# Kernel optimization log

Measured on AMD Instinct MI355X. Metric: run time of the kernel, lower is better.

Reference implementation:

```python
import jax, jax.numpy as jnp
import numpy as np

K = 32
D = 64
N_ITER = 10


def setup_inputs() -> dict:
    key = jax.random.key(0)
    k1, k2 = jax.random.split(key)
    B = 65536
    x = jax.random.normal(k1, (B, D), dtype=jnp.float32)
    c = jnp.zeros((K,), dtype=jnp.float32)
    mu = jax.random.normal(k2, (K, D), dtype=jnp.float32) * 0.1
    A = jnp.tile(jnp.eye(D, dtype=jnp.float32)[None], (K, 1, 1))
    alpha = jnp.float32(0.1)
    return {"x": x, "c": c, "mu": mu, "A": A, "alpha": alpha}


def _grad_phi(x, c, mu, A):
    # Precision matrices Sigma_i^{-1} = A_i^T A_i : (k, d, d)
    P = jnp.einsum('kji,kjl->kil', A, A)
    diff = x[:, None, :] - mu[None, :, :]          # (B, k, d)
    Pd = jnp.einsum('kij,bkj->bki', P, diff)       # Sigma^{-1} (x - mu)
    quad = jnp.einsum('bki,bki->bk', diff, Pd)     # (B, k)
    # Analytic gradient of phi(x) = logsumexp_i(c_i - 0.5 q_i):
    # grad = -sum_i softmax_i(c_i - 0.5 q_i) * Sigma_i^{-1}(x - mu_i)
    w = jax.nn.softmax(c[None, :] - 0.5 * quad, axis=1)  # (B, k)
    return -jnp.einsum('bk,bki->bi', w, Pd)


def reference(x, c, mu, A, alpha):
    def step(x_cur, _):
        x_new = x_cur + alpha * _grad_phi(x_cur, c, mu, A)
        return x_new, None
    x_final, _ = jax.lax.scan(step, x, None, length=N_ITER)
    return x_final
```

## Files before the change

kernel.cpp:

```cpp
#include <hip/hip_runtime.h>
#include <hip/hip_bf16.h>


typedef __attribute__((ext_vector_type(4))) float f32x4;
typedef __attribute__((ext_vector_type(8))) short bf16x8;

#define KC 32
#define NITER 10
#define XROW 72
#define WT_PITCH 40
#define PW_BYTES 7168
#define PSTG 8192
#define NBUF 4

static __device__ __forceinline__ unsigned pk_bf16(float a, float b) {
  __hip_bfloat16 ha = __float2bfloat16(a), hb = __float2bfloat16(b);
  unsigned short ua = *(unsigned short*)&ha, ub = *(unsigned short*)&hb;
  return (unsigned)ua | ((unsigned)ub << 16);
}

static __device__ __forceinline__ float red16(float x) {
#if __has_builtin(__builtin_amdgcn_permlane16_swap)
  int xi = __float_as_int(x);
  auto pr = __builtin_amdgcn_permlane16_swap(xi, xi, false, false);
  return __int_as_float(pr[0]) + __int_as_float(pr[1]);
#else
  int v = __builtin_amdgcn_ds_swizzle(__float_as_int(x), 0x401F);
  return x + __int_as_float(v);
#endif
}
static __device__ __forceinline__ float red32(float x) {
  int xi = __float_as_int(x);
  auto pr = __builtin_amdgcn_permlane32_swap(xi, xi, false, false);
  return __int_as_float(pr[0]) + __int_as_float(pr[1]);
}

static __device__ __forceinline__ void stage16(const void* gsrc, void* ldst) {
  __builtin_amdgcn_global_load_lds(
      (const __attribute__((address_space(1))) unsigned int*)gsrc,
      (__attribute__((address_space(3))) unsigned int*)ldst, 16, 0, 0);
}

__global__ void precompute1(const float* __restrict__ A, const float* __restrict__ mu,
                            const float* __restrict__ c,
                            float* __restrict__ Pmu_g, float* __restrict__ e_g,
                            __hip_bfloat16* __restrict__ Psw) {
  __shared__ float As[64 * 64];
  __shared__ float Pk[64 * 64];
  const int k = blockIdx.x, tid = threadIdx.x;
  const float* Ak = A + k * 4096;
  for (int idx = tid; idx < 1024; idx += 256)
    *(f32x4*)&As[idx * 4] = *(const f32x4*)&Ak[idx * 4];
  __syncthreads();

  const int i = tid >> 2, lg = tid & 3;
  float acc[16] = {};
  for (int j = 0; j < 64; ++j) {
    float ai = As[j * 64 + i];
    const f32x4* row = (const f32x4*)&As[j * 64 + lg * 16];
#pragma unroll
    for (int g = 0; g < 4; ++g) {
      f32x4 v = row[g];
#pragma unroll
      for (int r = 0; r < 4; ++r) acc[g * 4 + r] += ai * v[r];
    }
  }
#pragma unroll
  for (int g = 0; g < 4; ++g)
#pragma unroll
    for (int r = 0; r < 4; ++r) Pk[i * 64 + lg * 16 + g * 4 + r] = acc[g * 4 + r];
  __syncthreads();

  if (tid < 64) {
    float s = 0.f;
    for (int l = 0; l < 64; ++l) s += Pk[l * 64 + tid] * mu[k * 64 + l];
    Pmu_g[k * 64 + tid] = s;
    float v = mu[k * 64 + tid] * s;
#pragma unroll
    for (int off = 1; off < 64; off <<= 1) v += __shfl_xor(v, off, 64);
    if (tid == 0) e_g[k] = c[k] - 0.5f * v;
  }

  unsigned* Psw32 = (unsigned*)(Psw + k * 4096);
  for (int idx2 = tid; idx2 < 2048; idx2 += 256) {
    int idx = idx2 << 1;
    int f = idx >> 9, ln = (idx >> 3) & 63, j = idx & 7;
    int mt = f >> 1, s = f & 1, qq = ln >> 4, l4 = ln & 15;
    int col = mt * 16 + l4, rb = s * 32 + qq * 8 + j;
    Psw32[idx2] = pk_bf16(Pk[rb * 64 + col], Pk[(rb + 1) * 64 + col]);
  }
}

__global__ void precompute2(const float* __restrict__ Pmu_g,
                            __hip_bfloat16* __restrict__ PmuA,
                            __hip_bfloat16* __restrict__ PmuB) {
  const int tid = threadIdx.x;
  for (int idx = tid; idx < 2048; idx += 256) {
    int f = idx >> 9, lane = (idx >> 3) & 63, j = idx & 7;
    int mtc = f >> 1, s = f & 1, qq = lane >> 4, l4 = lane & 15;
    PmuA[idx] = __float2bfloat16(Pmu_g[(mtc * 16 + l4) * 64 + s * 32 + qq * 8 + j]);
  }
  for (int idx = tid; idx < 2048; idx += 256) {
    int f = idx >> 9, lane = (idx >> 3) & 63, j = idx & 7;
    int qq = lane >> 4, l4 = lane & 15;
    PmuB[idx] = __float2bfloat16(Pmu_g[(qq * 8 + j) * 64 + f * 16 + l4]);
  }
}

__launch_bounds__(256, 2)
__global__ void denoise_main(const float* __restrict__ x_in,
                             const float* __restrict__ e_g,
                             const float* __restrict__ alpha_g,
                             const __hip_bfloat16* __restrict__ Psw,
                             const __hip_bfloat16* __restrict__ PmuA,
                             const __hip_bfloat16* __restrict__ PmuB,
                             float* __restrict__ out) {
  __shared__ __attribute__((aligned(16))) char scratch[4 * PW_BYTES + NBUF * PSTG];

  const int tid = threadIdx.x;
  const int wave = tid >> 6, lane = tid & 63;
  const int q = lane >> 4, l4 = lane & 15;
  const int base_pt = blockIdx.x * 128 + wave * 32;
  const float alpha = alpha_g[0];

  char* pw = scratch + wave * PW_BYTES;
  __hip_bfloat16* xsw = (__hip_bfloat16*)pw;
  float* pmxw = (float*)pw;
  __hip_bfloat16* wtw = (__hip_bfloat16*)(pw + 4608);
  char* pstg = scratch + 4 * PW_BYTES;

  const char* PswB = (const char*)Psw;
  const bf16x8* PmuAF = (const bf16x8*)PmuA;
  const bf16x8* PmuBF = (const bf16x8*)PmuB;

  f32x4 xm[4][2];
#pragma unroll
  for (int mt = 0; mt < 4; ++mt)
#pragma unroll
    for (int nt = 0; nt < 2; ++nt)
      xm[mt][nt] = *(const f32x4*)&x_in[(base_pt + nt * 16 + l4) * 64 + mt * 16 + q * 4];

  f32x4 ev[2];
#pragma unroll
  for (int mtc = 0; mtc < 2; ++mtc) ev[mtc] = *(const f32x4*)&e_g[mtc * 16 + q * 4];

  const f32x4 Z4 = {0.f, 0.f, 0.f, 0.f};
  const int f0 = 2 * wave, f1 = 2 * wave + 1;

  stage16(PswB + f0 * 1024 + lane * 16, pstg + f0 * 1024);
  stage16(PswB + f1 * 1024 + lane * 16, pstg + f1 * 1024);
  stage16(PswB + PSTG + f0 * 1024 + lane * 16, pstg + PSTG + f0 * 1024);
  stage16(PswB + PSTG + f1 * 1024 + lane * 16, pstg + PSTG + f1 * 1024);

#pragma unroll 1
  for (int it = 0; it < NITER; ++it) {
#pragma unroll
    for (int mt = 0; mt < 4; ++mt)
#pragma unroll
      for (int nt = 0; nt < 2; ++nt) {
        uint2 v;
        v.x = pk_bf16(xm[mt][nt][0], xm[mt][nt][1]);
        v.y = pk_bf16(xm[mt][nt][2], xm[mt][nt][3]);
        *(uint2*)&xsw[(nt * 16 + l4) * XROW + mt * 16 + q * 4] = v;
      }

    bf16x8 bx[2][2];
#pragma unroll
    for (int s = 0; s < 2; ++s)
#pragma unroll
      for (int nt = 0; nt < 2; ++nt)
        bx[s][nt] = *(const bf16x8*)&xsw[(nt * 16 + l4) * XROW + s * 32 + q * 8];

    f32x4 pmx[2][2];
#pragma unroll
    for (int mtc = 0; mtc < 2; ++mtc)
#pragma unroll
      for (int nt = 0; nt < 2; ++nt)
        pmx[mtc][nt] =
            __builtin_amdgcn_mfma_f32_16x16x32_bf16(PmuAF[(mtc * 2) * 64 + lane], bx[0][nt], Z4, 0, 0, 0);
#pragma unroll
    for (int mtc = 0; mtc < 2; ++mtc)
#pragma unroll
      for (int nt = 0; nt < 2; ++nt)
        pmx[mtc][nt] = __builtin_amdgcn_mfma_f32_16x16x32_bf16(PmuAF[(mtc * 2 + 1) * 64 + lane],
                                                               bx[1][nt], pmx[mtc][nt], 0, 0, 0);
#pragma unroll
    for (int mtc = 0; mtc < 2; ++mtc)
#pragma unroll
      for (int nt = 0; nt < 2; ++nt)
#pragma unroll
        for (int r = 0; r < 4; ++r)
          pmxw[(mtc * 16 + q * 4 + r) * 32 + nt * 16 + l4] = pmx[mtc][nt][r] + ev[mtc][r];

    f32x4 accY[4][2];
#pragma unroll
    for (int mt = 0; mt < 4; ++mt)
#pragma unroll
      for (int nt = 0; nt < 2; ++nt) accY[mt][nt] = Z4;
    float lsum0 = 0.f, lsum1 = 0.f;

    asm volatile("s_waitcnt vmcnt(2)" ::: "memory");
    __builtin_amdgcn_s_barrier();
    asm volatile("" ::: "memory");

#pragma unroll 2
    for (int k = 0; k < KC; ++k) {
      {
        const int ks = (k + 2) & (KC - 1);
        const char* ps = PswB + ks * PSTG;
        char* pd = pstg + (ks & (NBUF - 1)) * PSTG;
        stage16(ps + f0 * 1024 + lane * 16, pd + f0 * 1024);
        stage16(ps + f1 * 1024 + lane * 16, pd + f1 * 1024);
      }

      const char* pc = pstg + (k & (NBUF - 1)) * PSTG;
      bf16x8 ap[4][2];
#pragma unroll
      for (int mt = 0; mt < 4; ++mt)
#pragma unroll
        for (int s = 0; s < 2; ++s)
          ap[mt][s] = *(const bf16x8*)(pc + (mt * 2 + s) * 1024 + lane * 16);

      f32x4 y[4][2];
#pragma unroll
      for (int mt = 0; mt < 4; ++mt)
#pragma unroll
        for (int nt = 0; nt < 2; ++nt)
          y[mt][nt] = __builtin_amdgcn_mfma_f32_16x16x32_bf16(ap[mt][0], bx[0][nt], Z4, 0, 0, 0);
#pragma unroll
      for (int mt = 0; mt < 4; ++mt)
#pragma unroll
        for (int nt = 0; nt < 2; ++nt)
          y[mt][nt] =
              __builtin_amdgcn_mfma_f32_16x16x32_bf16(ap[mt][1], bx[1][nt], y[mt][nt], 0, 0, 0);

      f32x4 d0 = xm[0][0] * y[0][0];
      f32x4 d1 = xm[0][1] * y[0][1];
#pragma unroll
      for (int mt = 1; mt < 4; ++mt) {
        d0 += xm[mt][0] * y[mt][0];
        d1 += xm[mt][1] * y[mt][1];
      }
      float xy0 = (d0[0] + d0[1]) + (d0[2] + d0[3]);
      float xy1 = (d1[0] + d1[1]) + (d1[2] + d1[3]);
      xy0 = red32(red16(xy0));
      xy1 = red32(red16(xy1));

      const float pk0 = pmxw[k * 32 + l4];
      const float pk1 = pmxw[k * 32 + 16 + l4];
      const float w0 = __expf(pk0 - 0.5f * xy0);
      const float w1 = __expf(pk1 - 0.5f * xy1);
      lsum0 += w0;
      lsum1 += w1;
      if (q == 0) {
        wtw[l4 * WT_PITCH + k] = __float2bfloat16(w0);
        wtw[(16 + l4) * WT_PITCH + k] = __float2bfloat16(w1);
      }
#pragma unroll
      for (int mt = 0; mt < 4; ++mt) {
        accY[mt][0] += w0 * y[mt][0];
        accY[mt][1] += w1 * y[mt][1];
      }

      asm volatile("s_waitcnt vmcnt(2)" ::: "memory");
      __builtin_amdgcn_s_barrier();
      asm volatile("" ::: "memory");
    }

    bf16x8 wtf[2];
#pragma unroll
    for (int nt = 0; nt < 2; ++nt)
      wtf[nt] = *(const bf16x8*)&wtw[(nt * 16 + l4) * WT_PITCH + q * 8];
    f32x4 pacc[4][2];
#pragma unroll
    for (int mt = 0; mt < 4; ++mt) {
      bf16x8 a = PmuBF[mt * 64 + lane];
      pacc[mt][0] = __builtin_amdgcn_mfma_f32_16x16x32_bf16(a, wtf[0], Z4, 0, 0, 0);
      pacc[mt][1] = __builtin_amdgcn_mfma_f32_16x16x32_bf16(a, wtf[1], Z4, 0, 0, 0);
    }

    const float c0 = alpha / lsum0;
    const float c1 = alpha / lsum1;
#pragma unroll
    for (int mt = 0; mt < 4; ++mt) {
      xm[mt][0] += c0 * (pacc[mt][0] - accY[mt][0]);
      xm[mt][1] += c1 * (pacc[mt][1] - accY[mt][1]);
    }
  }

#pragma unroll
  for (int mt = 0; mt < 4; ++mt)
#pragma unroll
    for (int nt = 0; nt < 2; ++nt)
      *(f32x4*)&out[(base_pt + nt * 16 + l4) * 64 + mt * 16 + q * 4] = xm[mt][nt];
}

extern "C" void kernel_launch(void* const* d_in, const int* in_sizes, int n_in,
                              void* d_out, int out_size, void* d_ws, size_t ws_size,
                              hipStream_t stream) {
  (void)in_sizes; (void)n_in; (void)out_size; (void)ws_size;
  const float* x = (const float*)d_in[0];
  const float* c = (const float*)d_in[1];
  const float* mu = (const float*)d_in[2];
  const float* A = (const float*)d_in[3];
  const float* alpha = (const float*)d_in[4];
  float* out = (float*)d_out;

  char* ws = (char*)d_ws;
  float* Pmu_g = (float*)(ws);
  float* e_g = (float*)(ws + 8192);
  __hip_bfloat16* PmuA = (__hip_bfloat16*)(ws + 8448);
  __hip_bfloat16* PmuB = (__hip_bfloat16*)(ws + 12544);
  __hip_bfloat16* Psw = (__hip_bfloat16*)(ws + 16640);

  precompute1<<<32, 256, 0, stream>>>(A, mu, c, Pmu_g, e_g, Psw);
  precompute2<<<1, 256, 0, stream>>>(Pmu_g, PmuA, PmuB);
  denoise_main<<<512, 256, 0, stream>>>(x, e_g, alpha, Psw, PmuA, PmuB, out);
}
```

Baseline: 292.8 us.

## Software-pipeline MFMA for next component with softmax chain of current

Restructures the per-component loop so the MFMA products for component k+1 are issued while the reduction/exp/accumulate chain for component k runs, using two ping-pong y register sets. The prefetch distance of the staged P matrices into LDS grows from 2 to 3 components (three initial stages), moved before the x loads. This aims to hide MFMA latency and the cross-lane reduction latency behind each other, at the cost of more VGPRs (double y buffers) and an unroll-1 loop that may limit scheduling.

```diff
diff --git a/kernel.cpp b/kernel.cpp
--- a/kernel.cpp
+++ b/kernel.cpp
@@ -133,6 +133,16 @@
   const bf16x8* PmuAF = (const bf16x8*)PmuA;
   const bf16x8* PmuBF = (const bf16x8*)PmuB;
 
+  const f32x4 Z4 = {0.f, 0.f, 0.f, 0.f};
+  const int f0 = 2 * wave, f1 = 2 * wave + 1;
+
+  stage16(PswB + 0 * PSTG + f0 * 1024 + lane * 16, pstg + 0 * PSTG + f0 * 1024);
+  stage16(PswB + 0 * PSTG + f1 * 1024 + lane * 16, pstg + 0 * PSTG + f1 * 1024);
+  stage16(PswB + 1 * PSTG + f0 * 1024 + lane * 16, pstg + 1 * PSTG + f0 * 1024);
+  stage16(PswB + 1 * PSTG + f1 * 1024 + lane * 16, pstg + 1 * PSTG + f1 * 1024);
+  stage16(PswB + 2 * PSTG + f0 * 1024 + lane * 16, pstg + 2 * PSTG + f0 * 1024);
+  stage16(PswB + 2 * PSTG + f1 * 1024 + lane * 16, pstg + 2 * PSTG + f1 * 1024);
+
   f32x4 xm[4][2];
 #pragma unroll
   for (int mt = 0; mt < 4; ++mt)
@@ -144,13 +154,71 @@
 #pragma unroll
   for (int mtc = 0; mtc < 2; ++mtc) ev[mtc] = *(const f32x4*)&e_g[mtc * 16 + q * 4];
 
-  const f32x4 Z4 = {0.f, 0.f, 0.f, 0.f};
-  const int f0 = 2 * wave, f1 = 2 * wave + 1;
-
-  stage16(PswB + f0 * 1024 + lane * 16, pstg + f0 * 1024);
-  stage16(PswB + f1 * 1024 + lane * 16, pstg + f1 * 1024);
-  stage16(PswB + PSTG + f0 * 1024 + lane * 16, pstg + PSTG + f0 * 1024);
-  stage16(PswB + PSTG + f1 * 1024 + lane * 16, pstg + PSTG + f1 * 1024);
+  f32x4 yA[4][2], yB[4][2];
+  f32x4 accY[4][2];
+  float lsum0, lsum1;
+  bf16x8 bx[2][2];
+
+  auto mfma_from = [&](f32x4(&y)[4][2], const char* pc) {
+    bf16x8 apr[4][2];
+#pragma unroll
+    for (int mt = 0; mt < 4; ++mt)
+#pragma unroll
+      for (int s = 0; s < 2; ++s)
+        apr[mt][s] = *(const bf16x8*)(pc + (mt * 2 + s) * 1024 + lane * 16);
+#pragma unroll
+    for (int mt = 0; mt < 4; ++mt)
+#pragma unroll
+      for (int nt = 0; nt < 2; ++nt)
+        y[mt][nt] = __builtin_amdgcn_mfma_f32_16x16x32_bf16(apr[mt][0], bx[0][nt], Z4, 0, 0, 0);
+#pragma unroll
+    for (int mt = 0; mt < 4; ++mt)
+#pragma unroll
+      for (int nt = 0; nt < 2; ++nt)
+        y[mt][nt] = __builtin_amdgcn_mfma_f32_16x16x32_bf16(apr[mt][1], bx[1][nt], y[mt][nt], 0, 0, 0);
+  };
+
+  auto chain = [&](const f32x4(&y)[4][2], int k) {
+    const float pk0 = pmxw[k * 32 + l4];
+    const float pk1 = pmxw[k * 32 + 16 + l4];
+    f32x4 d0 = xm[0][0] * y[0][0];
+    f32x4 d1 = xm[0][1] * y[0][1];
+#pragma unroll
+    for (int mt = 1; mt < 4; ++mt) {
+      d0 += xm[mt][0] * y[mt][0];
+      d1 += xm[mt][1] * y[mt][1];
+    }
+    float xy0 = (d0[0] + d0[1]) + (d0[2] + d0[3]);
+    float xy1 = (d1[0] + d1[1]) + (d1[2] + d1[3]);
+    xy0 = red32(red16(xy0));
+    xy1 = red32(red16(xy1));
+    const float w0 = __expf(pk0 - 0.5f * xy0);
+    const float w1 = __expf(pk1 - 0.5f * xy1);
+    lsum0 += w0;
+    lsum1 += w1;
+    if (q == 0) {
+      wtw[l4 * WT_PITCH + k] = __float2bfloat16(w0);
+      wtw[(16 + l4) * WT_PITCH + k] = __float2bfloat16(w1);
+    }
+#pragma unroll
+    for (int mt = 0; mt < 4; ++mt) {
+      accY[mt][0] += w0 * y[mt][0];
+      accY[mt][1] += w1 * y[mt][1];
+    }
+  };
+
+  auto stage_next = [&](int k) {
+    const int ks = (k + 3) & (KC - 1);
+    const char* ps = PswB + ks * PSTG;
+    char* pd = pstg + (ks & (NBUF - 1)) * PSTG;
+    stage16(ps + f0 * 1024 + lane * 16, pd + f0 * 1024);
+    stage16(ps + f1 * 1024 + lane * 16, pd + f1 * 1024);
+  };
+  auto syncstep = [&]() {
+    asm volatile("s_waitcnt vmcnt(2)" ::: "memory");
+    __builtin_amdgcn_s_barrier();
+    asm volatile("" ::: "memory");
+  };
 
 #pragma unroll 1
   for (int it = 0; it < NITER; ++it) {
@@ -164,7 +232,6 @@
         *(uint2*)&xsw[(nt * 16 + l4) * XROW + mt * 16 + q * 4] = v;
       }
 
-    bf16x8 bx[2][2];
 #pragma unroll
     for (int s = 0; s < 2; ++s)
 #pragma unroll
@@ -192,80 +259,35 @@
         for (int r = 0; r < 4; ++r)
           pmxw[(mtc * 16 + q * 4 + r) * 32 + nt * 16 + l4] = pmx[mtc][nt][r] + ev[mtc][r];
 
-    f32x4 accY[4][2];
 #pragma unroll
     for (int mt = 0; mt < 4; ++mt)
 #pragma unroll
       for (int nt = 0; nt < 2; ++nt) accY[mt][nt] = Z4;
-    float lsum0 = 0.f, lsum1 = 0.f;
-
-    asm volatile("s_waitcnt vmcnt(2)" ::: "memory");
-    __builtin_amdgcn_s_barrier();
-    asm volatile("" ::: "memory");
-
-#pragma unroll 2
-    for (int k = 0; k < KC; ++k) {
-      {
-        const int ks = (k + 2) & (KC - 1);
-        const char* ps = PswB + ks * PSTG;
-        char* pd = pstg + (ks & (NBUF - 1)) * PSTG;
-        stage16(ps + f0 * 1024 + lane * 16, pd + f0 * 1024);
-        stage16(ps + f1 * 1024 + lane * 16, pd + f1 * 1024);
-      }
-
-      const char* pc = pstg + (k & (NBUF - 1)) * PSTG;
-      bf16x8 ap[4][2];
-#pragma unroll
-      for (int mt = 0; mt < 4; ++mt)
-#pragma unroll
-        for (int s = 0; s < 2; ++s)
-          ap[mt][s] = *(const bf16x8*)(pc + (mt * 2 + s) * 1024 + lane * 16);
-
-      f32x4 y[4][2];
-#pragma unroll
-      for (int mt = 0; mt < 4; ++mt)
-#pragma unroll
-        for (int nt = 0; nt < 2; ++nt)
-          y[mt][nt] = __builtin_amdgcn_mfma_f32_16x16x32_bf16(ap[mt][0], bx[0][nt], Z4, 0, 0, 0);
-#pragma unroll
-      for (int mt = 0; mt < 4; ++mt)
-#pragma unroll
-        for (int nt = 0; nt < 2; ++nt)
-          y[mt][nt] =
-              __builtin_amdgcn_mfma_f32_16x16x32_bf16(ap[mt][1], bx[1][nt], y[mt][nt], 0, 0, 0);
-
-      f32x4 d0 = xm[0][0] * y[0][0];
-      f32x4 d1 = xm[0][1] * y[0][1];
-#pragma unroll
-      for (int mt = 1; mt < 4; ++mt) {
-        d0 += xm[mt][0] * y[mt][0];
-        d1 += xm[mt][1] * y[mt][1];
-      }
-      float xy0 = (d0[0] + d0[1]) + (d0[2] + d0[3]);
-      float xy1 = (d1[0] + d1[1]) + (d1[2] + d1[3]);
-      xy0 = red32(red16(xy0));
-      xy1 = red32(red16(xy1));
-
-      const float pk0 = pmxw[k * 32 + l4];
-      const float pk1 = pmxw[k * 32 + 16 + l4];
-      const float w0 = __expf(pk0 - 0.5f * xy0);
-      const float w1 = __expf(pk1 - 0.5f * xy1);
-      lsum0 += w0;
-      lsum1 += w1;
-      if (q == 0) {
-        wtw[l4 * WT_PITCH + k] = __float2bfloat16(w0);
-        wtw[(16 + l4) * WT_PITCH + k] = __float2bfloat16(w1);
-      }
-#pragma unroll
-      for (int mt = 0; mt < 4; ++mt) {
-        accY[mt][0] += w0 * y[mt][0];
-        accY[mt][1] += w1 * y[mt][1];
-      }
-
-      asm volatile("s_waitcnt vmcnt(2)" ::: "memory");
-      __builtin_amdgcn_s_barrier();
-      asm volatile("" ::: "memory");
-    }
+    lsum0 = 0.f;
+    lsum1 = 0.f;
+
+    syncstep();
+
+    mfma_from(yA, pstg + 0 * PSTG);
+#pragma unroll 1
+    for (int kp = 0; kp < 15; ++kp) {
+      const int kA = 2 * kp, kB = 2 * kp + 1;
+      stage_next(kA);
+      mfma_from(yB, pstg + ((kA + 1) & (NBUF - 1)) * PSTG);
+      chain(yA, kA);
+      syncstep();
+      stage_next(kB);
+      mfma_from(yA, pstg + ((kB + 1) & (NBUF - 1)) * PSTG);
+      chain(yB, kB);
+      syncstep();
+    }
+    stage_next(30);
+    mfma_from(yB, pstg + (31 & (NBUF - 1)) * PSTG);
+    chain(yA, 30);
+    syncstep();
+    stage_next(31);
+    chain(yB, 31);
+    syncstep();
 
     bf16x8 wtf[2];
 #pragma unroll
```

After: 312.0 us. 6.5% more time.
